# Kernel tuning notes

Hardware: AMD Instinct MI355X
Metric: run time of the kernel (lower is better)

The kernel has to match this reference:

```python
import jax, jax.numpy as jnp
import numpy as np

EMBED_DIM = 1024
NUM_HEADS = 16
HEAD_DIM = EMBED_DIM // NUM_HEADS


def setup_inputs() -> dict:
    key = jax.random.key(0)
    ks = jax.random.split(key, 9)
    B, P, E = 4, 1024, EMBED_DIM
    s = 1.0 / np.sqrt(E)
    return {
        "x": jax.random.normal(ks[0], (B, P, E), dtype=jnp.float32),
        "Wq": jax.random.normal(ks[1], (E, E), dtype=jnp.float32) * s,
        "bq": jnp.zeros((E,), dtype=jnp.float32),
        "Wk": jax.random.normal(ks[2], (E, E), dtype=jnp.float32) * s,
        "bk": jnp.zeros((E,), dtype=jnp.float32),
        "Wv": jax.random.normal(ks[3], (E, E), dtype=jnp.float32) * s,
        "bv": jnp.zeros((E,), dtype=jnp.float32),
        "Wo": jax.random.normal(ks[4], (E, E), dtype=jnp.float32) * s,
        "bo": jnp.zeros((E,), dtype=jnp.float32),
    }


def reference(x, Wq, bq, Wk, bk, Wv, bv, Wo, bo):
    B, P, E = x.shape
    A, D = NUM_HEADS, HEAD_DIM
    scale = jnp.asarray(np.sqrt(D), dtype=x.dtype)
    # torch Linear: y = x @ W.T + b
    q = (x @ Wq.T + bq).reshape(B, P, A, D).transpose(0, 2, 1, 3)  # (B,A,P,D)
    k = (x @ Wk.T + bk).reshape(B, P, A, D).transpose(0, 2, 1, 3)
    v = (x @ Wv.T + bv).reshape(B, P, A, D).transpose(0, 2, 1, 3)
    scores = jnp.einsum("bapd,baqd->bapq", q, k) / scale  # (B,A,P,P)
    attn = jax.nn.softmax(scores, axis=-1)
    out = jnp.einsum("bapq,baqd->bapd", attn, v)  # (B,A,P,D)
    out = out.transpose(0, 2, 1, 3).reshape(B, P, E)
    return out @ Wo.T + bo
```

## Files before the change

### kernel.cpp

```cpp
#include <hip/hip_runtime.h>
#include <stdint.h>

typedef unsigned short u16;
typedef short short4v __attribute__((ext_vector_type(4)));
typedef short short8v __attribute__((ext_vector_type(8)));
typedef float float4v __attribute__((ext_vector_type(4)));

#define AS1(p) ((__attribute__((address_space(1))) void*)(p))
#define AS3(p) ((__attribute__((address_space(3))) void*)(p))

#define MFMA32(a, b, c) __builtin_amdgcn_mfma_f32_16x16x32_bf16(a, b, c, 0, 0, 0)

static __device__ __forceinline__ float4v MFMA16(short4v a, short4v b, float4v c) {
#if __has_builtin(__builtin_amdgcn_mfma_f32_16x16x16bf16_1k)
  return __builtin_amdgcn_mfma_f32_16x16x16bf16_1k(a, b, c, 0, 0, 0);
#else
  float4v d;
  asm volatile("v_mfma_f32_16x16x16_bf16 %0, %1, %2, %3\n\ts_nop 7\n\ts_nop 3"
               : "=v"(d)
               : "v"(a), "v"(b), "v"(c));
  return d;
#endif
}

static __device__ __forceinline__ u16 f2bf(float f) {
  uint32_t u = __builtin_bit_cast(uint32_t, f);
  u += 0x7FFFu + ((u >> 16) & 1u);
  return (u16)(u >> 16);
}

static __device__ __forceinline__ unsigned cvtpk(float lo, float hi) {
  unsigned r;
  asm("v_cvt_pk_bf16_f32 %0, %1, %2" : "=v"(r) : "v"(lo), "v"(hi));
  return r;
}

#define TR4(v0_, v1_, v2_, v3_, addr_)                                   \
  asm volatile("ds_read_b64_tr_b16 %0, %4 offset:0\n\t"                  \
               "ds_read_b64_tr_b16 %1, %4 offset:2048\n\t"               \
               "ds_read_b64_tr_b16 %2, %4 offset:4096\n\t"               \
               "ds_read_b64_tr_b16 %3, %4 offset:6144\n\t"               \
               "s_waitcnt lgkmcnt(0)"                                    \
               : "=&v"(v0_), "=&v"(v1_), "=&v"(v2_), "=&v"(v3_)          \
               : "v"(addr_)                                              \
               : "memory")


__global__ __launch_bounds__(256) void cast1_k(const float* __restrict__ s, u16* __restrict__ d) {
  const int i = (blockIdx.x * 256 + threadIdx.x) * 4;
  float4v v = *(const float4v*)(s + i);
  short4v o;
#pragma unroll
  for (int j = 0; j < 4; j++) o[j] = (short)f2bf(v[j]);
  *(short4v*)(d + i) = o;
}

__global__ __launch_bounds__(256) void cast4_k(const float* __restrict__ s0, const float* __restrict__ s1,
                                               const float* __restrict__ s2, const float* __restrict__ s3,
                                               u16* __restrict__ d0, u16* __restrict__ d1,
                                               u16* __restrict__ d2, u16* __restrict__ d3) {
  const float* s;
  u16* d;
  switch (blockIdx.y) {
    case 0: s = s0; d = d0; break;
    case 1: s = s1; d = d1; break;
    case 2: s = s2; d = d2; break;
    default: s = s3; d = d3; break;
  }
  const int i = (blockIdx.x * 256 + threadIdx.x) * 4;
  float4v v = *(const float4v*)(s + i);
  short4v o;
#pragma unroll
  for (int j = 0; j < 4; j++) o[j] = (short)f2bf(v[j]);
  *(short4v*)(d + i) = o;
}


__global__ __launch_bounds__(512, 2) void gemm256(
    const u16* __restrict__ A,
    const u16* __restrict__ B0, const u16* __restrict__ B1, const u16* __restrict__ B2,
    const float* __restrict__ bias0, const float* __restrict__ bias1, const float* __restrict__ bias2,
    u16* __restrict__ C0, u16* __restrict__ C1, u16* __restrict__ C2,
    float sc0, float sc1, float sc2) {
  constexpr int K = 1024;
  __shared__ u16 As[4][256][32];
  __shared__ u16 Bs[4][256][32];

  const int t = threadIdx.x;
  const int lane = t & 63, wid = t >> 6;
  const int wm = wid >> 2, wn = wid & 3;
  const int lr = lane & 15, g = lane >> 4;

  const int id = blockIdx.x;
  const int xc = id & 7, off = id >> 3;
  const int mb = (xc & 3) * 4 + (off & 3);
  const int nbt = (xc >> 2) * 6 + (off >> 2);
  const int seg = nbt >> 2, nb = nbt & 3;

  const u16* Bm = seg == 0 ? B0 : (seg == 1 ? B1 : B2);
  const float* bias = seg == 0 ? bias0 : (seg == 1 ? bias1 : bias2);
  u16* C = seg == 0 ? C0 : (seg == 1 ? C1 : C2);
  const float scale = seg == 0 ? sc0 : (seg == 1 ? sc1 : sc2);

  const u16* Ap = A + (size_t)mb * 256 * K;
  const u16* Bp = Bm + (size_t)nb * 256 * K;

  float4v z = {0.f, 0.f, 0.f, 0.f};
  float4v acc[8][4];
#pragma unroll
  for (int i = 0; i < 8; i++)
#pragma unroll
    for (int j = 0; j < 4; j++) acc[i][j] = z;

  const int sr0 = t >> 2, sr1 = sr0 + 128;
  const int pc = (t & 3) * 8;
  const int scol = ((t & 3) ^ ((t >> 3) & 3)) * 8;

#define STGA(rg, kb)                                                                                            \
  {                                                                                                             \
    __builtin_amdgcn_global_load_lds(AS1(Ap + (size_t)sr0 * K + (kb) + scol), AS3(&As[rg][sr0][pc]), 16, 0, 0); \
    __builtin_amdgcn_global_load_lds(AS1(Ap + (size_t)sr1 * K + (kb) + scol), AS3(&As[rg][sr1][pc]), 16, 0, 0); \
  }
#define STGB(rg, kb)                                                                                            \
  {                                                                                                             \
    __builtin_amdgcn_global_load_lds(AS1(Bp + (size_t)sr0 * K + (kb) + scol), AS3(&Bs[rg][sr0][pc]), 16, 0, 0); \
    __builtin_amdgcn_global_load_lds(AS1(Bp + (size_t)sr1 * K + (kb) + scol), AS3(&Bs[rg][sr1][pc]), 16, 0, 0); \
  }
#define VM8 asm volatile("s_waitcnt vmcnt(8)" ::: "memory")
#define VM4 asm volatile("s_waitcnt vmcnt(4)" ::: "memory")
#define VM0 asm volatile("s_waitcnt vmcnt(0)" ::: "memory")

#define PH(rg, mq, STG_, VM_)                                                         \
  {                                                                                   \
    short8v a_[4], b_[4];                                                             \
    _Pragma("unroll") for (int i = 0; i < 4; i++) {                                   \
      const int r_ = wm * 128 + ((mq)*4 + i) * 16 + lr;                               \
      a_[i] = *(const short8v*)&As[rg][r_][(g ^ ((r_ >> 1) & 3)) * 8];                \
    }                                                                                 \
    _Pragma("unroll") for (int j = 0; j < 4; j++) {                                   \
      const int r_ = wn * 64 + j * 16 + lr;                                           \
      b_[j] = *(const short8v*)&Bs[rg][r_][(g ^ ((r_ >> 1) & 3)) * 8];                \
    }                                                                                 \
    STG_;                                                                             \
    VM_;                                                                              \
    __builtin_amdgcn_s_barrier();                                                     \
    asm volatile("s_waitcnt lgkmcnt(0)");                                             \
    __builtin_amdgcn_sched_barrier(0);                                                \
    __builtin_amdgcn_s_setprio(1);                                                    \
    _Pragma("unroll") for (int i = 0; i < 4; i++)                                     \
        _Pragma("unroll") for (int j = 0; j < 4; j++)                                 \
            acc[(mq)*4 + i][j] = MFMA32(a_[i], b_[j], acc[(mq)*4 + i][j]);            \
    __builtin_amdgcn_s_setprio(0);                                                    \
    __builtin_amdgcn_s_barrier();                                                     \
  }

  STGA(0, 0);
  STGB(0, 0);
  STGA(1, 32);
  STGB(1, 32);
  STGA(2, 64);
  STGB(2, 64);
  VM8;
  __builtin_amdgcn_s_barrier();

  for (int r = 0; r < 29; ++r) {
    const int rg = r & 3, rs = (r + 3) & 3, kb = (r + 3) * 32;
    PH(rg, 0, STGA(rs, kb), );
    PH(rg, 1, STGB(rs, kb), VM8);
  }
  PH(1, 0, , );
  PH(1, 1, , VM4);
  PH(2, 0, , );
  PH(2, 1, , VM0);
  PH(3, 0, , );
  PH(3, 1, , );

#undef PH
#undef STGA
#undef STGB

  const int colb = nb * 256 + wn * 64;
  const int rowb = mb * 256 + wm * 128;
#pragma unroll
  for (int j = 0; j < 4; j++) {
    const int col = colb + j * 16 + lr;
    const float bv = bias[col];
#pragma unroll
    for (int i = 0; i < 8; i++) {
      const int row0 = rowb + i * 16 + g * 4;
#pragma unroll
      for (int r = 0; r < 4; r++)
        C[(size_t)(row0 + r) * 1024 + col] = f2bf((acc[i][j][r] + bv) * scale);
    }
  }
}


template <int OUTF32>
__global__ __launch_bounds__(256) void gemm_bt(
    const u16* __restrict__ A,
    const u16* __restrict__ B0, const u16* __restrict__ B1, const u16* __restrict__ B2,
    const float* __restrict__ bias0, const float* __restrict__ bias1, const float* __restrict__ bias2,
    void* __restrict__ C0, void* __restrict__ C1, void* __restrict__ C2,
    float sc0, float sc1, float sc2) {
  constexpr int K = 1024;
  __shared__ u16 As[2][128 * 32];
  __shared__ u16 Bs[2][128 * 32];

  const int t = threadIdx.x;
  const int lane = t & 63, wid = t >> 6;
  const int wr = wid >> 1, wc = wid & 1;
  const int lr = lane & 15, g = lane >> 4;

  const int seg = blockIdx.y >> 3, nb = blockIdx.y & 7, mb = blockIdx.x;
  const u16* B = seg == 0 ? B0 : (seg == 1 ? B1 : B2);
  const float* bias = seg == 0 ? bias0 : (seg == 1 ? bias1 : bias2);
  void* C = seg == 0 ? C0 : (seg == 1 ? C1 : C2);
  const float scale = seg == 0 ? sc0 : (seg == 1 ? sc1 : sc2);

  const u16* Ap = A + (size_t)mb * 128 * K;
  const u16* Bp = B + (size_t)nb * 128 * K;

  float4v z = {0.f, 0.f, 0.f, 0.f};
  float4v acc[4][4];
#pragma unroll
  for (int i = 0; i < 4; i++)
#pragma unroll
    for (int j = 0; j < 4; j++) acc[i][j] = z;

  const int r0 = t >> 2, c0 = (t & 3) * 8;

#define GSTAGE(u, kk)                                                                                          \
  do {                                                                                                         \
    __builtin_amdgcn_global_load_lds(AS1(Ap + (size_t)r0 * K + (kk) + c0), AS3(&As[u][t * 8]), 16, 0, 0);      \
    __builtin_amdgcn_global_load_lds(AS1(Ap + (size_t)(r0 + 64) * K + (kk) + c0), AS3(&As[u][(t + 256) * 8]),  \
                                     16, 0, 0);                                                                \
    __builtin_amdgcn_global_load_lds(AS1(Bp + (size_t)r0 * K + (kk) + c0), AS3(&Bs[u][t * 8]), 16, 0, 0);      \
    __builtin_amdgcn_global_load_lds(AS1(Bp + (size_t)(r0 + 64) * K + (kk) + c0), AS3(&Bs[u][(t + 256) * 8]),  \
                                     16, 0, 0);                                                                \
  } while (0)

  GSTAGE(0, 0);
  int cur = 0;
  for (int k0 = 0; k0 < K; k0 += 32) {
    __syncthreads();
    if (k0 + 32 < K) GSTAGE(cur ^ 1, k0 + 32);

    const u16* Au = &As[cur][0];
    const u16* Bu = &Bs[cur][0];
    short8v af[4], bfr[4];
#pragma unroll
    for (int mi = 0; mi < 4; mi++) af[mi] = *(const short8v*)(Au + (wr * 64 + mi * 16 + lr) * 32 + g * 8);
#pragma unroll
    for (int ni = 0; ni < 4; ni++) bfr[ni] = *(const short8v*)(Bu + (wc * 64 + ni * 16 + lr) * 32 + g * 8);
    __builtin_amdgcn_s_setprio(1);
#pragma unroll
    for (int mi = 0; mi < 4; mi++)
#pragma unroll
      for (int ni = 0; ni < 4; ni++) acc[mi][ni] = MFMA32(af[mi], bfr[ni], acc[mi][ni]);
    __builtin_amdgcn_s_setprio(0);
    __syncthreads();
    cur ^= 1;
  }
#undef GSTAGE

  const int colb = nb * 128 + wc * 64;
  const int rowb = mb * 128 + wr * 64;
#pragma unroll
  for (int ni = 0; ni < 4; ni++) {
    const int col = colb + ni * 16 + lr;
    const float bv = bias[col];
#pragma unroll
    for (int mi = 0; mi < 4; mi++) {
      const int row0 = rowb + mi * 16 + g * 4;
      float4v a = acc[mi][ni];
      if (OUTF32) {
        float* Cf = (float*)C;
#pragma unroll
        for (int r = 0; r < 4; r++) Cf[(size_t)(row0 + r) * 1024 + col] = (a[r] + bv) * scale;
      } else {
        u16* Cb = (u16*)C;
#pragma unroll
        for (int r = 0; r < 4; r++) Cb[(size_t)(row0 + r) * 1024 + col] = f2bf((a[r] + bv) * scale);
      }
    }
  }
}


__global__ __launch_bounds__(256) void attn_fwd(const u16* __restrict__ Qm, const u16* __restrict__ Km,
                                                const u16* __restrict__ Vm, u16* __restrict__ Om) {
  __shared__ u16 Ks[2][64 * 64];
  __shared__ u16 Vs[2][64 * 64];

  const int t = threadIdx.x;
  const int lane = t & 63, w = t >> 6;
  const int lr = lane & 15, g = lane >> 4;
  const int qb = blockIdx.x, pair = blockIdx.y;
  const int b = pair >> 4, a = pair & 15;

  const int qrow = qb * 64 + w * 16 + lr;
  const size_t qoff = ((size_t)(b * 1024 + qrow)) * 1024 + a * 64;
  const short8v qf0 = *(const short8v*)(Qm + qoff + g * 8);
  const short8v qf1 = *(const short8v*)(Qm + qoff + 32 + g * 8);

  float4v z = {0.f, 0.f, 0.f, 0.f};
  float4v ot[4];
#pragma unroll
  for (int i = 0; i < 4; i++) ot[i] = z;
  float mrun = -3.0e38f, lsum = 0.f;

  const u16* Kb = Km + ((size_t)b * 1024) * 1024 + a * 64;
  const u16* Vb = Vm + ((size_t)b * 1024) * 1024 + a * 64;

  const int kr0 = t >> 3, kr1 = kr0 + 32;
  const int kc0 = ((t & 7) ^ (kr0 & 7)) * 8;
  const int vr0 = (t >> 1) & 63;
  const int vc0 = (t >> 7) * 16 + (t & 1) * 8;

#define ASTAGE(u, kt)                                                                                             \
  do {                                                                                                            \
    __builtin_amdgcn_global_load_lds(AS1(Kb + (size_t)((kt) + kr0) * 1024 + kc0), AS3(&Ks[u][t * 8]), 16, 0, 0);  \
    __builtin_amdgcn_global_load_lds(AS1(Kb + (size_t)((kt) + kr1) * 1024 + kc0), AS3(&Ks[u][(t + 256) * 8]),     \
                                     16, 0, 0);                                                                   \
    __builtin_amdgcn_global_load_lds(AS1(Vb + (size_t)((kt) + vr0) * 1024 + vc0), AS3(&Vs[u][t * 8]), 16, 0, 0);  \
    __builtin_amdgcn_global_load_lds(AS1(Vb + (size_t)((kt) + vr0) * 1024 + vc0 + 32), AS3(&Vs[u][(t + 256) * 8]),\
                                     16, 0, 0);                                                                   \
  } while (0)

  const unsigned vsbase = (unsigned)(uintptr_t)AS3(&Vs[0][0]);
  const unsigned vlane = (unsigned)((g * 4 + (lr >> 2)) * 32 + (lane & 3) * 8);

  ASTAGE(0, 0);
  int cur = 0;
  for (int kt = 0; kt < 1024; kt += 64) {
    __syncthreads();
    if (kt + 64 < 1024) ASTAGE(cur ^ 1, kt + 64);

    const u16* Ku = &Ks[cur][0];
    float4v st[4];
#pragma unroll
    for (int jt = 0; jt < 4; jt++) {
      float4v s = z;
      const int row = jt * 16 + lr;
      const int rsw = (row & 7) << 4;
      __builtin_amdgcn_s_setprio(1);
#pragma unroll
      for (int ks = 0; ks < 2; ks++) {
        const int baddr = (row * 128 + (ks * 4 + g) * 16) ^ rsw;
        short8v kf = *(const short8v*)((const char*)Ku + baddr);
        s = MFMA32(kf, ks ? qf1 : qf0, s);
      }
      __builtin_amdgcn_s_setprio(0);
      st[jt] = s;
    }

    float tm = st[0][0];
#pragma unroll
    for (int jt = 0; jt < 4; jt++)
#pragma unroll
      for (int r = 0; r < 4; r++) tm = fmaxf(tm, st[jt][r]);
    tm = fmaxf(tm, __shfl_xor(tm, 16));
    tm = fmaxf(tm, __shfl_xor(tm, 32));
    if (!__all(tm - mrun <= 8.f)) {
      const float mnew = fmaxf(mrun, tm);
      const float sca = exp2f(mrun - mnew);
      lsum *= sca;
#pragma unroll
      for (int d = 0; d < 4; d++)
#pragma unroll
        for (int r = 0; r < 4; r++) ot[d][r] *= sca;
      mrun = mnew;
    }
    float p[16];
    float ts = 0.f;
#pragma unroll
    for (int jt = 0; jt < 4; jt++)
#pragma unroll
      for (int r = 0; r < 4; r++) {
        const float pv = exp2f(st[jt][r] - mrun);
        p[jt * 4 + r] = pv;
        ts += pv;
      }
    ts += __shfl_xor(ts, 16);
    ts += __shfl_xor(ts, 32);
    lsum += ts;

    short4v pf[4];
#pragma unroll
    for (int jt = 0; jt < 4; jt++) {
      unsigned lo = cvtpk(p[jt * 4 + 0], p[jt * 4 + 1]);
      unsigned hi = cvtpk(p[jt * 4 + 2], p[jt * 4 + 3]);
      unsigned u2[2] = {lo, hi};
      pf[jt] = __builtin_bit_cast(short4v, *(unsigned long long*)u2);
    }

    unsigned va = vsbase + (unsigned)cur * 8192u + vlane;
#pragma unroll
    for (int jt = 0; jt < 4; jt++) {
      short4v vf0, vf1, vf2, vf3;
      TR4(vf0, vf1, vf2, vf3, va);
      __builtin_amdgcn_s_setprio(1);
      ot[0] = MFMA16(vf0, pf[jt], ot[0]);
      ot[1] = MFMA16(vf1, pf[jt], ot[1]);
      ot[2] = MFMA16(vf2, pf[jt], ot[2]);
      ot[3] = MFMA16(vf3, pf[jt], ot[3]);
      __builtin_amdgcn_s_setprio(0);
      va += 512u;
    }

    __syncthreads();
    cur ^= 1;
  }
#undef ASTAGE

  const float inv = 1.f / lsum;
  u16* Op = Om + ((size_t)(b * 1024 + qrow)) * 1024 + a * 64;
#pragma unroll
  for (int dblk = 0; dblk < 4; dblk++) {
    short4v o4;
#pragma unroll
    for (int r = 0; r < 4; r++) o4[r] = (short)f2bf(ot[dblk][r] * inv);
    *(short4v*)(Op + dblk * 16 + g * 4) = o4;
  }
}


extern "C" void kernel_launch(void* const* d_in, const int* in_sizes, int n_in,
                              void* d_out, int out_size, void* d_ws, size_t ws_size,
                              hipStream_t stream) {
  (void)in_sizes; (void)n_in; (void)out_size; (void)ws_size;
  const float* x = (const float*)d_in[0];
  const float* Wq = (const float*)d_in[1];
  const float* bq = (const float*)d_in[2];
  const float* Wk = (const float*)d_in[3];
  const float* bk = (const float*)d_in[4];
  const float* Wv = (const float*)d_in[5];
  const float* bv = (const float*)d_in[6];
  const float* Wo = (const float*)d_in[7];
  const float* bo = (const float*)d_in[8];
  float* out = (float*)d_out;

  char* ws = (char*)d_ws;
  const size_t MB = 1u << 20;
  u16* xb = (u16*)(ws + 0 * MB);
  u16* Wqb = (u16*)(ws + 8 * MB);
  u16* Wkb = (u16*)(ws + 10 * MB);
  u16* Wvb = (u16*)(ws + 12 * MB);
  u16* Wob = (u16*)(ws + 14 * MB);
  u16* Qb = (u16*)(ws + 16 * MB);
  u16* Kb = (u16*)(ws + 24 * MB);
  u16* Vb = (u16*)(ws + 32 * MB);
  u16* Ab = (u16*)(ws + 40 * MB);

  const float csc = 1.4426950408889634f / 8.0f;

  cast1_k<<<4096, 256, 0, stream>>>(x, xb);
  cast4_k<<<dim3(1024, 4), 256, 0, stream>>>(Wq, Wk, Wv, Wo, Wqb, Wkb, Wvb, Wob);
  gemm256<<<192, 512, 0, stream>>>(xb, Wqb, Wkb, Wvb, bq, bk, bv, Qb, Kb, Vb, csc, 1.f, 1.f);
  attn_fwd<<<dim3(16, 64), 256, 0, stream>>>(Qb, Kb, Vb, Ab);
  gemm_bt<1><<<dim3(32, 8), 256, 0, stream>>>(Ab, Wob, Wob, Wob, bo, bo, bo, out, out, out, 1.f, 1.f, 1.f);
}
```

Before: 195.4 us.

## Triple-buffer K/V tiles and software-pipeline QK^T with PV in attention

The attention kernel moves from double to triple LDS buffering of the K/V tiles. Its loop is restructured so the QK^T MFMAs for the next tile are issued alongside the PV MFMAs of the current tile, with softmax placed in between. The __syncthreads calls become raw s_barrier with explicit vmcnt waits, so up to two tiles of global-to-LDS loads stay in flight. The goal is to hide load latency and the softmax critical path behind matrix math, at the cost of more LDS per block and fragile manual waitcnt bookkeeping.

```diff
diff --git a/kernel.cpp b/kernel.cpp
--- a/kernel.cpp
+++ b/kernel.cpp
@@ -44,6 +44,9 @@
                : "=&v"(v0_), "=&v"(v1_), "=&v"(v2_), "=&v"(v3_)          \
                : "v"(addr_)                                              \
                : "memory")
+
+#define ABAR() asm volatile("s_barrier" ::: "memory")
+#define AVBAR(N) asm volatile("s_waitcnt vmcnt(" #N ")\n\ts_barrier" ::: "memory")
 
 
 __global__ __launch_bounds__(256) void cast1_k(const float* __restrict__ s, u16* __restrict__ d) {
@@ -290,8 +293,8 @@
 
 __global__ __launch_bounds__(256) void attn_fwd(const u16* __restrict__ Qm, const u16* __restrict__ Km,
                                                 const u16* __restrict__ Vm, u16* __restrict__ Om) {
-  __shared__ u16 Ks[2][64 * 64];
-  __shared__ u16 Vs[2][64 * 64];
+  __shared__ u16 Ks[3][64 * 64];
+  __shared__ u16 Vs[3][64 * 64];
 
   const int t = threadIdx.x;
   const int lane = t & 63, w = t >> 6;
@@ -331,88 +334,109 @@
   const unsigned vsbase = (unsigned)(uintptr_t)AS3(&Vs[0][0]);
   const unsigned vlane = (unsigned)((g * 4 + (lr >> 2)) * 32 + (lane & 3) * 8);
 
+  float4v st[4];
+  short4v pf[4];
+
+#define AQKT(rc)                                                                 \
+  {                                                                              \
+    const char* Kbase = (const char*)&Ks[rc][0];                                 \
+    __builtin_amdgcn_s_setprio(1);                                               \
+    _Pragma("unroll") for (int jt = 0; jt < 4; jt++) {                           \
+      const int row = jt * 16 + lr;                                              \
+      const int rsw = (row & 7) << 4;                                            \
+      short8v kf0 = *(const short8v*)(Kbase + ((row * 128 + g * 16) ^ rsw));     \
+      short8v kf1 = *(const short8v*)(Kbase + ((row * 128 + (4 + g) * 16) ^ rsw));\
+      float4v s = MFMA32(kf0, qf0, z);                                           \
+      s = MFMA32(kf1, qf1, s);                                                   \
+      st[jt] = s;                                                                \
+    }                                                                            \
+    __builtin_amdgcn_s_setprio(0);                                               \
+  }
+
+#define ASM_()                                                                   \
+  {                                                                              \
+    float m0 = fmaxf(fmaxf(st[0][0], st[0][1]), fmaxf(st[0][2], st[0][3]));      \
+    float m1 = fmaxf(fmaxf(st[1][0], st[1][1]), fmaxf(st[1][2], st[1][3]));      \
+    float m2 = fmaxf(fmaxf(st[2][0], st[2][1]), fmaxf(st[2][2], st[2][3]));      \
+    float m3 = fmaxf(fmaxf(st[3][0], st[3][1]), fmaxf(st[3][2], st[3][3]));      \
+    float tm = fmaxf(fmaxf(m0, m1), fmaxf(m2, m3));                              \
+    tm = fmaxf(tm, __shfl_xor(tm, 16));                                          \
+    tm = fmaxf(tm, __shfl_xor(tm, 32));                                          \
+    if (!__all(tm - mrun <= 8.f)) {                                              \
+      const float mnew = fmaxf(mrun, tm);                                        \
+      const float sca = exp2f(mrun - mnew);                                      \
+      lsum *= sca;                                                               \
+      _Pragma("unroll") for (int d = 0; d < 4; d++)                              \
+          _Pragma("unroll") for (int r = 0; r < 4; r++) ot[d][r] *= sca;         \
+      mrun = mnew;                                                               \
+    }                                                                            \
+    float p[16];                                                                 \
+    _Pragma("unroll") for (int jt = 0; jt < 4; jt++)                             \
+        _Pragma("unroll") for (int r = 0; r < 4; r++)                            \
+            p[jt * 4 + r] = exp2f(st[jt][r] - mrun);                             \
+    float q0 = (p[0] + p[1]) + (p[2] + p[3]);                                    \
+    float q1 = (p[4] + p[5]) + (p[6] + p[7]);                                    \
+    float q2 = (p[8] + p[9]) + (p[10] + p[11]);                                  \
+    float q3 = (p[12] + p[13]) + (p[14] + p[15]);                                \
+    float ts = (q0 + q1) + (q2 + q3);                                            \
+    ts += __shfl_xor(ts, 16);                                                    \
+    ts += __shfl_xor(ts, 32);                                                    \
+    lsum += ts;                                                                  \
+    _Pragma("unroll") for (int jt = 0; jt < 4; jt++) {                           \
+      unsigned lo = cvtpk(p[jt * 4 + 0], p[jt * 4 + 1]);                         \
+      unsigned hi = cvtpk(p[jt * 4 + 2], p[jt * 4 + 3]);                         \
+      unsigned u2[2] = {lo, hi};                                                 \
+      pf[jt] = __builtin_bit_cast(short4v, *(unsigned long long*)u2);            \
+    }                                                                            \
+  }
+
+#define APV(rc)                                                                  \
+  {                                                                              \
+    unsigned va = vsbase + (unsigned)(rc)*8192u + vlane;                         \
+    _Pragma("unroll") for (int jt = 0; jt < 4; jt++) {                           \
+      short4v vf0, vf1, vf2, vf3;                                                \
+      TR4(vf0, vf1, vf2, vf3, va);                                               \
+      __builtin_amdgcn_s_setprio(1);                                             \
+      ot[0] = MFMA16(vf0, pf[jt], ot[0]);                                        \
+      ot[1] = MFMA16(vf1, pf[jt], ot[1]);                                        \
+      ot[2] = MFMA16(vf2, pf[jt], ot[2]);                                        \
+      ot[3] = MFMA16(vf3, pf[jt], ot[3]);                                        \
+      __builtin_amdgcn_s_setprio(0);                                             \
+      va += 512u;                                                                \
+    }                                                                            \
+  }
+
   ASTAGE(0, 0);
-  int cur = 0;
-  for (int kt = 0; kt < 1024; kt += 64) {
-    __syncthreads();
-    if (kt + 64 < 1024) ASTAGE(cur ^ 1, kt + 64);
-
-    const u16* Ku = &Ks[cur][0];
-    float4v st[4];
-#pragma unroll
-    for (int jt = 0; jt < 4; jt++) {
-      float4v s = z;
-      const int row = jt * 16 + lr;
-      const int rsw = (row & 7) << 4;
-      __builtin_amdgcn_s_setprio(1);
-#pragma unroll
-      for (int ks = 0; ks < 2; ks++) {
-        const int baddr = (row * 128 + (ks * 4 + g) * 16) ^ rsw;
-        short8v kf = *(const short8v*)((const char*)Ku + baddr);
-        s = MFMA32(kf, ks ? qf1 : qf0, s);
-      }
-      __builtin_amdgcn_s_setprio(0);
-      st[jt] = s;
-    }
-
-    float tm = st[0][0];
-#pragma unroll
-    for (int jt = 0; jt < 4; jt++)
-#pragma unroll
-      for (int r = 0; r < 4; r++) tm = fmaxf(tm, st[jt][r]);
-    tm = fmaxf(tm, __shfl_xor(tm, 16));
-    tm = fmaxf(tm, __shfl_xor(tm, 32));
-    if (!__all(tm - mrun <= 8.f)) {
-      const float mnew = fmaxf(mrun, tm);
-      const float sca = exp2f(mrun - mnew);
-      lsum *= sca;
-#pragma unroll
-      for (int d = 0; d < 4; d++)
-#pragma unroll
-        for (int r = 0; r < 4; r++) ot[d][r] *= sca;
-      mrun = mnew;
-    }
-    float p[16];
-    float ts = 0.f;
-#pragma unroll
-    for (int jt = 0; jt < 4; jt++)
-#pragma unroll
-      for (int r = 0; r < 4; r++) {
-        const float pv = exp2f(st[jt][r] - mrun);
-        p[jt * 4 + r] = pv;
-        ts += pv;
-      }
-    ts += __shfl_xor(ts, 16);
-    ts += __shfl_xor(ts, 32);
-    lsum += ts;
-
-    short4v pf[4];
-#pragma unroll
-    for (int jt = 0; jt < 4; jt++) {
-      unsigned lo = cvtpk(p[jt * 4 + 0], p[jt * 4 + 1]);
-      unsigned hi = cvtpk(p[jt * 4 + 2], p[jt * 4 + 3]);
-      unsigned u2[2] = {lo, hi};
-      pf[jt] = __builtin_bit_cast(short4v, *(unsigned long long*)u2);
-    }
-
-    unsigned va = vsbase + (unsigned)cur * 8192u + vlane;
-#pragma unroll
-    for (int jt = 0; jt < 4; jt++) {
-      short4v vf0, vf1, vf2, vf3;
-      TR4(vf0, vf1, vf2, vf3, va);
-      __builtin_amdgcn_s_setprio(1);
-      ot[0] = MFMA16(vf0, pf[jt], ot[0]);
-      ot[1] = MFMA16(vf1, pf[jt], ot[1]);
-      ot[2] = MFMA16(vf2, pf[jt], ot[2]);
-      ot[3] = MFMA16(vf3, pf[jt], ot[3]);
-      __builtin_amdgcn_s_setprio(0);
-      va += 512u;
-    }
-
-    __syncthreads();
-    cur ^= 1;
-  }
+  ASTAGE(1, 64);
+  ASTAGE(2, 128);
+  AVBAR(8);
+  AQKT(0);
+  ASM_();
+  AVBAR(4);
+
+  for (int tt = 0; tt < 13; ++tt) {
+    const int rc = tt % 3, rn = (tt + 1) % 3;
+    AQKT(rn);
+    APV(rc);
+    ABAR();
+    ASTAGE(rc, (tt + 3) * 64);
+    ASM_();
+    AVBAR(4);
+  }
+  AQKT(2);
+  APV(1);
+  ABAR();
+  ASM_();
+  AVBAR(0);
+  AQKT(0);
+  APV(2);
+  ASM_();
+  APV(0);
+
 #undef ASTAGE
+#undef AQKT
+#undef ASM_
+#undef APV
 
   const float inv = 1.f / lsum;
   u16* Op = Om + ((size_t)(b * 1024 + qrow)) * 1024 + a * 64;
```

New measurement: 197.2 us. About the same (+1.0%).
